# Kernel optimization log

Measured on AMD Instinct MI355X. Metric: run time of the kernel, lower is better.

Reference implementation:

```python
import jax, jax.numpy as jnp
import numpy as np

EPS_LN = 1e-6
EPS_NORM = 1e-12
MAX_SCALE_MUL = float(np.log(100.0))
H = 16  # num_heads


def _ln(x):
    # affine-free LayerNorm over last dim (torch uses biased variance)
    mu = jnp.mean(x, axis=-1, keepdims=True)
    var = jnp.mean((x - mu) ** 2, axis=-1, keepdims=True)
    return (x - mu) / jnp.sqrt(var + EPS_LN)


def _l2norm(x):
    n = jnp.sqrt(jnp.sum(x * x, axis=-1, keepdims=True))
    return x / jnp.maximum(n, EPS_NORM)


def setup_inputs() -> dict:
    key = jax.random.key(0)
    ks = jax.random.split(key, 12)
    B, L, C = 4, 1024, 1024
    Ccond, Dff = 1024, 4096
    s = lambda fan: 1.0 / np.sqrt(fan)
    return {
        "x": jax.random.normal(ks[0], (B, L, C), jnp.float32),
        "cond": jax.random.normal(ks[1], (B, Ccond), jnp.float32),
        "mat_qkv_w": jax.random.normal(ks[2], (3 * C, C), jnp.float32) * s(C),
        "q_bias": jnp.zeros((C,), jnp.float32),
        "v_bias": jnp.zeros((C,), jnp.float32),
        "scale_mul": jnp.full((1, H, 1, 1), np.log(4.0), jnp.float32),
        "proj_w": jax.random.normal(ks[3], (C, C), jnp.float32) * s(C),
        "proj_b": jnp.zeros((C,), jnp.float32),
        "ada_w": jax.random.normal(ks[4], (6 * C, Ccond), jnp.float32) * s(Ccond),
        "ada_b": jnp.zeros((6 * C,), jnp.float32),
        "fc1_w": jax.random.normal(ks[5], (Dff, C), jnp.float32) * s(C),
        "fc1_b": jnp.zeros((Dff,), jnp.float32),
        "fc2_w": jax.random.normal(ks[6], (C, Dff), jnp.float32) * s(Dff),
        "fc2_b": jnp.zeros((C,), jnp.float32),
    }


def reference(x, cond, mat_qkv_w, q_bias, v_bias, scale_mul, proj_w, proj_b,
              ada_w, ada_b, fc1_w, fc1_b, fc2_w, fc2_b):
    B, L, C = x.shape
    hd = C // H

    # AdaLN modulation params: SiLU -> Linear -> [B,1,6,C]
    ada = jax.nn.silu(cond) @ ada_w.T + ada_b
    ada = ada.reshape(B, 1, 6, C)
    gamma1, gamma2, scale1, scale2, shift1, shift2 = [ada[:, :, i] for i in range(6)]

    # --- attention branch ---
    x1 = _ln(x) * (scale1 + 1.0) + shift1
    qkv_bias = jnp.concatenate([q_bias, jnp.zeros_like(q_bias), v_bias])
    qkv = (x1 @ mat_qkv_w.T + qkv_bias).reshape(B, L, 3, H, hd)
    q, k, v = [jnp.transpose(qkv[:, :, i], (0, 2, 1, 3)) for i in range(3)]  # [B,H,L,hd]

    sm = jnp.exp(jnp.minimum(scale_mul, MAX_SCALE_MUL))  # [1,H,1,1]
    q = _l2norm(q) * sm
    k = _l2norm(k)

    scores = jnp.einsum('bhqd,bhkd->bhqk', q, k)  # scale = 1.0 under l2 norm
    probs = jax.nn.softmax(scores, axis=-1)
    o = jnp.einsum('bhqk,bhkd->bhqd', probs, v)
    o = jnp.transpose(o, (0, 2, 1, 3)).reshape(B, L, C)
    attn_out = o @ proj_w.T + proj_b
    x = x + attn_out * gamma1

    # --- FFN branch ---
    x2 = _ln(x) * (scale2 + 1.0) + shift2
    h = jax.nn.gelu(x2 @ fc1_w.T + fc1_b, approximate=False)
    ffn_out = h @ fc2_w.T + fc2_b
    x = x + ffn_out * gamma2
    return x
```

## Files before the change

### kernel.cpp

```cpp
#include <hip/hip_runtime.h>

typedef __bf16 bf16x8_t __attribute__((ext_vector_type(8)));
typedef bf16x8_t bf16x8 __attribute__((may_alias));
typedef float f32x4 __attribute__((ext_vector_type(4)));
typedef unsigned short u16x4 __attribute__((ext_vector_type(4)));
typedef unsigned short u16x8 __attribute__((ext_vector_type(8)));

#define DEV __device__ __forceinline__

DEV float b2f(unsigned short u) {
  union { unsigned int i; float f; } x; x.i = ((unsigned int)u) << 16; return x.f;
}
DEV unsigned short f2b(float f) {
  union { float f; unsigned int i; } x; x.f = f;
  return (unsigned short)((x.i + 0x7fffu + ((x.i >> 16) & 1u)) >> 16);
}

#define AS1(p) ((__attribute__((address_space(1))) void*)(p))
#define AS3(p) ((__attribute__((address_space(3))) void*)(p))

__global__ void k_silu(const float* __restrict__ c, float* __restrict__ o) {
  int i = blockIdx.x * 256 + threadIdx.x;
  float v = c[i];
  o[i] = v / (1.f + __expf(-v));
}

__global__ __launch_bounds__(256) void k_ada(const float* __restrict__ sc,
                                             const float* __restrict__ w,
                                             const float* __restrict__ bias,
                                             float* __restrict__ out) {
  int j = blockIdx.x * 4 + (threadIdx.x >> 6);
  int lane = threadIdx.x & 63;
  const float* wr = w + (size_t)j * 1024;
  float s0 = 0.f, s1 = 0.f, s2 = 0.f, s3 = 0.f;
#pragma unroll
  for (int u = 0; u < 4; ++u) {
    int k = u * 256 + lane * 4;
    float4 a = *(const float4*)(wr + k);
    float4 c0 = *(const float4*)(sc + k);
    float4 c1 = *(const float4*)(sc + 1024 + k);
    float4 c2 = *(const float4*)(sc + 2048 + k);
    float4 c3 = *(const float4*)(sc + 3072 + k);
    s0 += a.x * c0.x + a.y * c0.y + a.z * c0.z + a.w * c0.w;
    s1 += a.x * c1.x + a.y * c1.y + a.z * c1.z + a.w * c1.w;
    s2 += a.x * c2.x + a.y * c2.y + a.z * c2.z + a.w * c2.w;
    s3 += a.x * c3.x + a.y * c3.y + a.z * c3.z + a.w * c3.w;
  }
#pragma unroll
  for (int o = 1; o < 64; o <<= 1) {
    s0 += __shfl_xor(s0, o); s1 += __shfl_xor(s1, o);
    s2 += __shfl_xor(s2, o); s3 += __shfl_xor(s3, o);
  }
  if (lane == 0) {
    float bb = bias[j];
    out[j] = s0 + bb;
    out[6144 + j] = s1 + bb;
    out[12288 + j] = s2 + bb;
    out[18432 + j] = s3 + bb;
  }
}

__global__ void k_cast(const float* __restrict__ s, unsigned short* __restrict__ d, int n) {
  int i = (blockIdx.x * 256 + threadIdx.x) * 4;
  if (i >= n) return;
  float4 v = *(const float4*)(s + i);
  u16x4 o;
  o[0] = f2b(v.x); o[1] = f2b(v.y); o[2] = f2b(v.z); o[3] = f2b(v.w);
  *(u16x4*)(d + i) = o;
}

__global__ __launch_bounds__(256) void k_ln_mod(const float* __restrict__ src,
                                                const float* __restrict__ ada,
                                                unsigned short* __restrict__ dst,
                                                int sidx, int hidx) {
  int row = blockIdx.x;
  int b = row >> 10;
  int t = threadIdx.x, lane = t & 63, wv = t >> 6;
  float4 v = *(const float4*)(src + (size_t)row * 1024 + t * 4);
  float s = v.x + v.y + v.z + v.w;
  float s2 = v.x * v.x + v.y * v.y + v.z * v.z + v.w * v.w;
#pragma unroll
  for (int o = 1; o < 64; o <<= 1) { s += __shfl_xor(s, o); s2 += __shfl_xor(s2, o); }
  __shared__ float red[8];
  if (lane == 0) { red[wv] = s; red[4 + wv] = s2; }
  __syncthreads();
  float ts = red[0] + red[1] + red[2] + red[3];
  float ts2 = red[4] + red[5] + red[6] + red[7];
  float mu = ts * (1.f / 1024.f);
  float var = ts2 * (1.f / 1024.f) - mu * mu;
  float rstd = rsqrtf(var + 1e-6f);
  const float* ar = ada + (size_t)b * 6144;
  float4 sc = *(const float4*)(ar + sidx * 1024 + t * 4);
  float4 sh = *(const float4*)(ar + hidx * 1024 + t * 4);
  u16x4 o;
  o[0] = f2b((v.x - mu) * rstd * (sc.x + 1.f) + sh.x);
  o[1] = f2b((v.y - mu) * rstd * (sc.y + 1.f) + sh.y);
  o[2] = f2b((v.z - mu) * rstd * (sc.z + 1.f) + sh.z);
  o[3] = f2b((v.w - mu) * rstd * (sc.w + 1.f) + sh.w);
  *(u16x4*)(dst + (size_t)row * 1024 + t * 4) = o;
}

template <int EPI, int SPLIT>
__global__ __launch_bounds__(512, 2) void k_gemm256(const unsigned short* __restrict__ A,
                                                    const unsigned short* __restrict__ W,
                                                    int N, int lda, int ldb, int nt,
                                                    const float* __restrict__ bias,
                                                    const float* __restrict__ qb,
                                                    const float* __restrict__ vb,
                                                    unsigned short* __restrict__ o0,
                                                    unsigned short* __restrict__ o1,
                                                    unsigned short* __restrict__ o2,
                                                    unsigned short* __restrict__ o3) {
  __shared__ unsigned short LDS[65536];
  const int tid = threadIdx.x;
  const int wv = tid >> 6, lane = tid & 63;
  const int fr = lane & 15, fg = lane >> 4;
  const int wm = wv >> 2, wn = wv & 3;

  const int cpx = gridDim.x >> 3;
  int wid = ((int)blockIdx.x & 7) * cpx + ((int)blockIdx.x >> 3);
  int s = 0;
  if (SPLIT > 1) { s = wid & (SPLIT - 1); wid >>= 2; }
  const int nx = N >> 8;
  const int m0 = (wid / nx) * 256, n0 = (wid % nx) * 256;
  const int kbase = s * (nt << 6);
  unsigned short* outp = (SPLIT > 1) ? (s == 0 ? o0 : s == 1 ? o1 : s == 2 ? o2 : o3) : o0;

  const int sRow = lane >> 2;
  const int sCh = (lane & 3) ^ ((lane >> 3) & 3);
  const unsigned short* aG = A + (size_t)(m0 + wv * 16 + sRow) * lda + kbase + sCh * 8;
  const unsigned short* bG = W + (size_t)(n0 + wv * 16 + sRow) * ldb + kbase + sCh * 8;

#define STQ(qi_, iop_, rh_)                                                                   \
  __builtin_amdgcn_global_load_lds(                                                          \
      AS1(((iop_) ? bG : aG) + (size_t)(rh_)*128 * ((iop_) ? ldb : lda) +                    \
          (((qi_) >> 1) * 64 + ((qi_)&1) * 32)),                                             \
      AS3(LDS + ((qi_)&3) * 16384 + (iop_)*8192 + (rh_)*4096 + wv * 512), 16, 0, 0)

  const int rswz = (fr >> 1) & 3;
  const int aRd = (wm * 128 + fr) * 32 + ((fg ^ rswz) << 3);
  const int bRd = 8192 + (wn * 64 + fr) * 32 + ((fg ^ rswz) << 3);

  f32x4 zz = {0.f, 0.f, 0.f, 0.f};
  f32x4 acc[8][4];
#pragma unroll
  for (int i = 0; i < 8; ++i)
#pragma unroll
    for (int j = 0; j < 4; ++j) acc[i][j] = zz;

#pragma unroll
  for (int qq = 0; qq < 3; ++qq) {
    STQ(qq, 0, 0); STQ(qq, 0, 1); STQ(qq, 1, 0); STQ(qq, 1, 1);
  }
  asm volatile("s_waitcnt vmcnt(8)" ::: "memory");
  __builtin_amdgcn_s_barrier();

#define LDSV(off) (*(const bf16x8*)(LDS + (off)))

  for (int t = 0; t < nt; ++t) {
    bf16x8 bq0, bq1, bq2, bq3;
#pragma unroll
    for (int p = 0; p < 4; ++p) {
      const int kk = p >> 1;
      const int reg = ((2 * t + kk) & 3) * 16384;
      if ((p & 1) == 0) {
        bq0 = LDSV(reg + bRd);
        bq1 = LDSV(reg + bRd + 512);
        bq2 = LDSV(reg + bRd + 1024);
        bq3 = LDSV(reg + bRd + 1536);
      }
      bf16x8 a0 = LDSV(reg + aRd + (p & 1) * 2048);
      bf16x8 a1 = LDSV(reg + aRd + (p & 1) * 2048 + 512);
      bf16x8 a2 = LDSV(reg + aRd + (p & 1) * 2048 + 1024);
      bf16x8 a3 = LDSV(reg + aRd + (p & 1) * 2048 + 1536);
      {
        const int gph = 4 * t + p;
        const int qi = (gph >> 1) + 3;
        if (qi < 2 * nt) {
          const int iop = gph & 1;
          if (iop) { STQ(qi, 1, 0); STQ(qi, 1, 1); }
          else     { STQ(qi, 0, 0); STQ(qi, 0, 1); }
        }
      }
      __builtin_amdgcn_s_barrier();
      asm volatile("s_waitcnt lgkmcnt(0)" ::: "memory");
      __builtin_amdgcn_sched_barrier(0);
      __builtin_amdgcn_s_setprio(1);
      const int mg = (p & 1) * 4;
#pragma unroll
      for (int ni = 0; ni < 4; ++ni) {
        bf16x8 bb = ni == 0 ? bq0 : ni == 1 ? bq1 : ni == 2 ? bq2 : bq3;
        acc[mg + 0][ni] = __builtin_amdgcn_mfma_f32_16x16x32_bf16(a0, bb, acc[mg + 0][ni], 0, 0, 0);
        acc[mg + 1][ni] = __builtin_amdgcn_mfma_f32_16x16x32_bf16(a1, bb, acc[mg + 1][ni], 0, 0, 0);
        acc[mg + 2][ni] = __builtin_amdgcn_mfma_f32_16x16x32_bf16(a2, bb, acc[mg + 2][ni], 0, 0, 0);
        acc[mg + 3][ni] = __builtin_amdgcn_mfma_f32_16x16x32_bf16(a3, bb, acc[mg + 3][ni], 0, 0, 0);
      }
      __builtin_amdgcn_s_setprio(0);
      if (p == 1) {
        if (t == nt - 1) { asm volatile("s_waitcnt vmcnt(0)" ::: "memory"); }
        else             { asm volatile("s_waitcnt vmcnt(8)" ::: "memory"); }
      } else if (p == 3 && t < nt - 1) {
        if (t == nt - 2) { asm volatile("s_waitcnt vmcnt(4)" ::: "memory"); }
        else             { asm volatile("s_waitcnt vmcnt(8)" ::: "memory"); }
      }
      __builtin_amdgcn_s_barrier();
    }
  }

#pragma unroll
  for (int mi = 0; mi < 8; ++mi) {
#pragma unroll
    for (int ni = 0; ni < 4; ++ni) {
#pragma unroll
      for (int r = 0; r < 4; ++r) {
        int m = m0 + wm * 128 + mi * 16 + fg * 4 + r;
        int n = n0 + wn * 64 + ni * 16 + fr;
        float v = acc[mi][ni][r];
        if constexpr (EPI == 0) {
          float bb = (n < 1024) ? qb[n] : ((n < 2048) ? 0.f : vb[n - 2048]);
          outp[(size_t)m * N + n] = f2b(v + bb);
        } else if constexpr (EPI == 2) {
          float z = v + bias[n];
          float u = z * (0.7978845608f + 0.0356774081f * z * z);
          float e = __expf(2.f * u);
          float th = 1.f - 2.f / (e + 1.f);
          outp[(size_t)m * N + n] = f2b(0.5f * z * (1.f + th));
        } else {
          outp[(size_t)m * N + n] = f2b(v);
        }
      }
    }
  }
#undef STQ
#undef LDSV
}

__global__ __launch_bounds__(256) void k_fc2red(const unsigned short* __restrict__ P0,
                                                const unsigned short* __restrict__ P1,
                                                const unsigned short* __restrict__ P2,
                                                const unsigned short* __restrict__ P3,
                                                const float* __restrict__ xmid,
                                                const float* __restrict__ bias,
                                                const float* __restrict__ ada,
                                                float* __restrict__ out) {
  size_t idx = ((size_t)blockIdx.x * 256 + threadIdx.x) * 8;
  int n = (int)(idx & 1023);
  int b = (int)(idx >> 20);
  u16x8 v0 = *(const u16x8*)(P0 + idx);
  u16x8 v1 = *(const u16x8*)(P1 + idx);
  u16x8 v2 = *(const u16x8*)(P2 + idx);
  u16x8 v3 = *(const u16x8*)(P3 + idx);
  const float* gp = ada + (size_t)b * 6144 + 1024 + n;
  const float* bp = bias + n;
  const float* xp = xmid + idx;
  float* op = out + idx;
#pragma unroll
  for (int i = 0; i < 8; ++i) {
    float sum = b2f(v0[i]) + b2f(v1[i]) + b2f(v2[i]) + b2f(v3[i]);
    op[i] = xp[i] + (sum + bp[i]) * gp[i];
  }
}

__global__ __launch_bounds__(512) void k_gemm8(const unsigned short* __restrict__ A,
                                               const unsigned short* __restrict__ W,
                                               int M, int N, int K, int Khalf,
                                               const float* __restrict__ bias,
                                               const float* __restrict__ resid,
                                               const float* __restrict__ ada,
                                               float* __restrict__ outp) {
  __shared__ unsigned short SM[49152];
  const int t = threadIdx.x, lane = t & 63, wv = t >> 6;
  const int grp = wv >> 2, w4 = wv & 3;
  const int wr = w4 >> 1, wc = w4 & 1;
  const int cpx = gridDim.x >> 3;
  const int orig = blockIdx.x;
  const int wid = (orig & 7) * cpx + (orig >> 3);
  const int nx = N >> 7;
  const int m0 = (wid / nx) * 128, n0 = (wid % nx) * 128;

  f32x4 zz = {0.f, 0.f, 0.f, 0.f};
  f32x4 acc[4][4];
#pragma unroll
  for (int i = 0; i < 4; ++i)
#pragma unroll
    for (int j = 0; j < 4; ++j) acc[i][j] = zz;

  const int srow = lane >> 2, scol = (lane & 3) * 8;
  const int kbase = grp * Khalf;
  const unsigned short* aSrc0 = A + (size_t)(m0 + w4 * 16 + srow) * K + kbase + scol;
  const unsigned short* aSrc1 = aSrc0 + (size_t)64 * K;
  const unsigned short* bSrc0 = W + (size_t)(n0 + w4 * 16 + srow) * K + kbase + scol;
  const unsigned short* bSrc1 = bSrc0 + (size_t)64 * K;
  unsigned short* grpA = SM + grp * 24576;

  const int fr = lane & 15, fk = (lane >> 4) * 8;

#define STG8(buf_, k0_)                                                                            \
  {                                                                                                \
    __builtin_amdgcn_global_load_lds(AS1(aSrc0 + (k0_)), AS3(grpA + (buf_)*8192 + w4 * 512), 16, 0, 0); \
    __builtin_amdgcn_global_load_lds(AS1(aSrc1 + (k0_)), AS3(grpA + (buf_)*8192 + 2048 + w4 * 512), 16, 0, 0); \
    __builtin_amdgcn_global_load_lds(AS1(bSrc0 + (k0_)), AS3(grpA + (buf_)*8192 + 4096 + w4 * 512), 16, 0, 0); \
    __builtin_amdgcn_global_load_lds(AS1(bSrc1 + (k0_)), AS3(grpA + (buf_)*8192 + 6144 + w4 * 512), 16, 0, 0); \
  }

  const int nsteps = Khalf >> 5;
  STG8(0, 0);
  STG8(1, 32);
  asm volatile("s_waitcnt vmcnt(4)" ::: "memory");
  __builtin_amdgcn_s_barrier();

  for (int i = 0; i < nsteps; ++i) {
    const int buf = i % 3;
    if (i + 2 < nsteps) STG8((i + 2) % 3, (i + 2) * 32);
    const unsigned short* aRd = grpA + buf * 8192 + (wr * 64 + fr) * 32 + fk;
    const unsigned short* bRd = grpA + buf * 8192 + 4096 + (wc * 64 + fr) * 32 + fk;
    bf16x8 af[4], bfv[4];
#pragma unroll
    for (int q = 0; q < 4; ++q) af[q] = *(const bf16x8*)(aRd + q * 512);
#pragma unroll
    for (int q = 0; q < 4; ++q) bfv[q] = *(const bf16x8*)(bRd + q * 512);
#pragma unroll
    for (int mi = 0; mi < 4; ++mi)
#pragma unroll
      for (int ni = 0; ni < 4; ++ni)
        acc[mi][ni] = __builtin_amdgcn_mfma_f32_16x16x32_bf16(af[mi], bfv[ni], acc[mi][ni], 0, 0, 0);
    if (i < nsteps - 1) {
      if (i + 2 < nsteps) {
        asm volatile("s_waitcnt vmcnt(4)" ::: "memory");
      } else {
        asm volatile("s_waitcnt vmcnt(0)" ::: "memory");
      }
      __builtin_amdgcn_s_barrier();
    }
  }
  __syncthreads();

  float* xch = (float*)SM;
#pragma unroll
  for (int c = 0; c < 16; ++c) {
    if (grp == 1)
      *(f32x4*)&xch[c * 1024 + (w4 * 64 + lane) * 4] = acc[c >> 2][c & 3];
  }
  __syncthreads();
  if (grp == 1) return;
#pragma unroll
  for (int c = 0; c < 16; ++c) {
    f32x4 p = *(const f32x4*)&xch[c * 1024 + (w4 * 64 + lane) * 4];
    acc[c >> 2][c & 3] += p;
  }

  const int fg = lane >> 4;
#pragma unroll
  for (int mi = 0; mi < 4; ++mi) {
#pragma unroll
    for (int ni = 0; ni < 4; ++ni) {
#pragma unroll
      for (int r = 0; r < 4; ++r) {
        int m = m0 + wr * 64 + mi * 16 + fg * 4 + r;
        int n = n0 + wc * 64 + ni * 16 + fr;
        float v = acc[mi][ni][r];
        float g = ada[(size_t)(m >> 10) * 6144 + n];
        outp[(size_t)m * N + n] = resid[(size_t)m * N + n] + (v + bias[n]) * g;
      }
    }
  }
#undef STG8
}

__global__ __launch_bounds__(256) void k_qknorm(const unsigned short* __restrict__ qkv,
                                                const float* __restrict__ smul,
                                                unsigned short* __restrict__ Qn,
                                                unsigned short* __restrict__ Kn) {
  int row = blockIdx.x;
  int b = row >> 10, l = row & 1023;
  int t = threadIdx.x;
  int h = t >> 4, sl = t & 15;
  const unsigned short* base = qkv + (size_t)row * 3072 + h * 64 + sl * 4;
  size_t off = ((size_t)(b * 16 + h) * 1024 + l) * 64 + sl * 4;
  {
    u16x4 qv = *(const u16x4*)base;
    float q0 = b2f(qv[0]), q1 = b2f(qv[1]), q2 = b2f(qv[2]), q3 = b2f(qv[3]);
    float ss = q0 * q0 + q1 * q1 + q2 * q2 + q3 * q3;
#pragma unroll
    for (int o = 1; o < 16; o <<= 1) ss += __shfl_xor(ss, o);
    float sm = __expf(fminf(smul[h], 4.6051701859880914f));
    float qs = sm / fmaxf(sqrtf(ss), 1e-12f);
    u16x4 o; o[0] = f2b(q0 * qs); o[1] = f2b(q1 * qs); o[2] = f2b(q2 * qs); o[3] = f2b(q3 * qs);
    *(u16x4*)(Qn + off) = o;
  }
  {
    u16x4 kv = *(const u16x4*)(base + 1024);
    float k0 = b2f(kv[0]), k1 = b2f(kv[1]), k2 = b2f(kv[2]), k3 = b2f(kv[3]);
    float ss = k0 * k0 + k1 * k1 + k2 * k2 + k3 * k3;
#pragma unroll
    for (int o = 1; o < 16; o <<= 1) ss += __shfl_xor(ss, o);
    float ks = 1.f / fmaxf(sqrtf(ss), 1e-12f);
    u16x4 o; o[0] = f2b(k0 * ks); o[1] = f2b(k1 * ks); o[2] = f2b(k2 * ks); o[3] = f2b(k3 * ks);
    *(u16x4*)(Kn + off) = o;
  }
}

__global__ __launch_bounds__(256) void k_vtrans(const unsigned short* __restrict__ qkv,
                                                unsigned short* __restrict__ Vt) {
  int bh = blockIdx.y, b = bh >> 4, h = bh & 15;
  int l0 = blockIdx.x * 64;
  __shared__ unsigned short tile[64][72];
  int t = threadIdx.x;
  int lr = t >> 2, dp = (t & 3) * 16;
  const unsigned short* src = qkv + (size_t)(b * 1024 + l0 + lr) * 3072 + 2048 + h * 64 + dp;
  *(u16x8*)&tile[lr][dp] = *(const u16x8*)src;
  *(u16x8*)&tile[lr][dp + 8] = *(const u16x8*)(src + 8);
  __syncthreads();
  int d = t >> 2, lp = (t & 3) * 16;
  unsigned short ov[16];
#pragma unroll
  for (int j = 0; j < 16; ++j) {
    int p = lp + j;
    int l = ((p >> 5) * 2 + ((p >> 2) & 1)) * 16 + ((p >> 3) & 3) * 4 + (p & 3);
    ov[j] = tile[l][d];
  }
  unsigned short* dst = Vt + ((size_t)bh * 64 + d) * 1024 + l0 + lp;
  *(u16x8*)dst = *(u16x8*)&ov[0];
  *(u16x8*)(dst + 8) = *(u16x8*)&ov[8];
}

__global__ __launch_bounds__(256) void k_attn(const unsigned short* __restrict__ Qn,
                                              const unsigned short* __restrict__ Kn,
                                              const unsigned short* __restrict__ Vt,
                                              const float* __restrict__ smul,
                                              unsigned short* __restrict__ O) {
  const int qt = blockIdx.x, bh = blockIdx.y;
  const int b = bh >> 4, h = bh & 15;
  const int t = threadIdx.x, lane = t & 63, wv = t >> 6;
  const int fr = lane & 15, fg = lane >> 4;
  __shared__ unsigned short Kb[2][4096];
  __shared__ unsigned short Vb[2][4096];

  const int q0 = qt * 128 + wv * 32;
  const unsigned short* qp = Qn + ((size_t)bh * 1024 + q0 + fr) * 64 + fg * 8;
  bf16x8 qf00 = *(const bf16x8*)qp;
  bf16x8 qf01 = *(const bf16x8*)(qp + 32);
  bf16x8 qf10 = *(const bf16x8*)(qp + 1024);
  bf16x8 qf11 = *(const bf16x8*)(qp + 1024 + 32);

  const float M = __expf(fminf(smul[h], 4.6051701859880914f));

  const int srow = lane >> 3, sc = lane & 7;
  const int xr = (sc ^ srow) * 8;
  const unsigned short* kp0 = Kn + (size_t)bh * 65536 + (size_t)(wv * 16 + srow) * 64 + xr;
  const unsigned short* kp1 = kp0 + 8 * 64;
  const unsigned short* vp0 = Vt + (size_t)bh * 65536 + (size_t)(wv * 16 + srow) * 1024 + xr;
  const unsigned short* vp1 = vp0 + 8 * 1024;

  f32x4 zz = {0.f, 0.f, 0.f, 0.f};
  f32x4 oa0[4], oa1[4];
#pragma unroll
  for (int i = 0; i < 4; ++i) { oa0[i] = zz; oa1[i] = zz; }
  float ls0 = 0.f, ls1 = 0.f;

  {
    unsigned short* kd = &Kb[0][wv * 1024];
    unsigned short* vd = &Vb[0][wv * 1024];
    __builtin_amdgcn_global_load_lds(AS1(kp0), AS3(kd), 16, 0, 0);
    __builtin_amdgcn_global_load_lds(AS1(kp1), AS3(kd + 512), 16, 0, 0);
    __builtin_amdgcn_global_load_lds(AS1(vp0), AS3(vd), 16, 0, 0);
    __builtin_amdgcn_global_load_lds(AS1(vp1), AS3(vd + 512), 16, 0, 0);
  }
  __syncthreads();

  int cur = 0;
  for (int kv = 0; kv < 1024; kv += 64) {
    const int nxt = cur ^ 1;
    if (kv + 64 < 1024) {
      const int ko = (kv + 64) * 64;
      const int vo = kv + 64;
      unsigned short* kd = &Kb[nxt][wv * 1024];
      unsigned short* vd = &Vb[nxt][wv * 1024];
      __builtin_amdgcn_global_load_lds(AS1(kp0 + ko), AS3(kd), 16, 0, 0);
      __builtin_amdgcn_global_load_lds(AS1(kp1 + ko), AS3(kd + 512), 16, 0, 0);
      __builtin_amdgcn_global_load_lds(AS1(vp0 + vo), AS3(vd), 16, 0, 0);
      __builtin_amdgcn_global_load_lds(AS1(vp1 + vo), AS3(vd + 512), 16, 0, 0);
    }

    f32x4 s0[4], s1[4];
#pragma unroll
    for (int ct = 0; ct < 4; ++ct) {
      const int row = ct * 16 + fr, r7 = row & 7;
      const unsigned short* kr = &Kb[cur][row * 64];
      bf16x8 kf0 = *(const bf16x8*)(kr + ((fg ^ r7) << 3));
      bf16x8 kf1 = *(const bf16x8*)(kr + (((4 + fg) ^ r7) << 3));
      f32x4 z0 = __builtin_amdgcn_mfma_f32_16x16x32_bf16(kf0, qf00, zz, 0, 0, 0);
      s0[ct] = __builtin_amdgcn_mfma_f32_16x16x32_bf16(kf1, qf01, z0, 0, 0, 0);
      f32x4 z1 = __builtin_amdgcn_mfma_f32_16x16x32_bf16(kf0, qf10, zz, 0, 0, 0);
      s1[ct] = __builtin_amdgcn_mfma_f32_16x16x32_bf16(kf1, qf11, z1, 0, 0, 0);
    }

    bf16x8 pa0[2], pa1[2];
#pragma unroll
    for (int kg = 0; kg < 2; ++kg) {
      bf16x8 a0, a1;
#pragma unroll
      for (int c2 = 0; c2 < 2; ++c2) {
#pragma unroll
        for (int r = 0; r < 4; ++r) {
          float e0 = __expf(s0[kg * 2 + c2][r] - M);
          float e1 = __expf(s1[kg * 2 + c2][r] - M);
          ls0 += e0; ls1 += e1;
          a0[c2 * 4 + r] = (__bf16)e0;
          a1[c2 * 4 + r] = (__bf16)e1;
        }
      }
      pa0[kg] = a0; pa1[kg] = a1;
    }

#pragma unroll
    for (int kg = 0; kg < 2; ++kg) {
#pragma unroll
      for (int dt = 0; dt < 4; ++dt) {
        const int row = dt * 16 + fr, r7 = row & 7;
        bf16x8 vf = *(const bf16x8*)(&Vb[cur][row * 64] + ((((kg << 2) + fg) ^ r7) << 3));
        oa0[dt] = __builtin_amdgcn_mfma_f32_16x16x32_bf16(pa0[kg], vf, oa0[dt], 0, 0, 0);
        oa1[dt] = __builtin_amdgcn_mfma_f32_16x16x32_bf16(pa1[kg], vf, oa1[dt], 0, 0, 0);
      }
    }
    __syncthreads();
    cur = nxt;
  }

  ls0 += __shfl_xor(ls0, 16); ls0 += __shfl_xor(ls0, 32);
  ls1 += __shfl_xor(ls1, 16); ls1 += __shfl_xor(ls1, 32);

#pragma unroll
  for (int r = 0; r < 4; ++r) {
    float i0 = 1.f / __shfl(ls0, fg * 4 + r);
    float i1 = 1.f / __shfl(ls1, fg * 4 + r);
    unsigned short* ob = O + ((size_t)(b * 1024 + q0 + fg * 4 + r)) * 1024 + h * 64 + fr;
#pragma unroll
    for (int dt = 0; dt < 4; ++dt) {
      ob[dt * 16] = f2b(oa0[dt][r] * i0);
      ob[(size_t)16 * 1024 + dt * 16] = f2b(oa1[dt][r] * i1);
    }
  }
}

extern "C" void kernel_launch(void* const* d_in, const int* in_sizes, int n_in,
                              void* d_out, int out_size, void* d_ws, size_t ws_size,
                              hipStream_t stream) {
  const float* x        = (const float*)d_in[0];
  const float* cond     = (const float*)d_in[1];
  const float* qkv_w    = (const float*)d_in[2];
  const float* q_bias   = (const float*)d_in[3];
  const float* v_bias   = (const float*)d_in[4];
  const float* scale_mul= (const float*)d_in[5];
  const float* proj_w   = (const float*)d_in[6];
  const float* proj_b   = (const float*)d_in[7];
  const float* ada_w    = (const float*)d_in[8];
  const float* ada_b    = (const float*)d_in[9];
  const float* fc1_w    = (const float*)d_in[10];
  const float* fc1_b    = (const float*)d_in[11];
  const float* fc2_w    = (const float*)d_in[12];
  const float* fc2_b    = (const float*)d_in[13];
  float* out = (float*)d_out;
  char* ws = (char*)d_ws;

  unsigned short* WQ   = (unsigned short*)(ws + 0);
  unsigned short* WP   = (unsigned short*)(ws + 6291456);
  unsigned short* WF1  = (unsigned short*)(ws + 8388608);
  unsigned short* WF2  = (unsigned short*)(ws + 16777216);
  float*          SIL  = (float*)(ws + 25165824);
  float*          ADA  = (float*)(ws + 25182208);
  unsigned short* X1   = (unsigned short*)(ws + 25280512);
  unsigned short* QKVB = (unsigned short*)(ws + 33669120);
  unsigned short* QN   = (unsigned short*)(ws + 58834944);
  unsigned short* KN   = (unsigned short*)(ws + 67223552);
  unsigned short* VT   = (unsigned short*)(ws + 75612160);
  unsigned short* OB   = (unsigned short*)(ws + 84000768);
  float*          XMID = (float*)(ws + 33669120);
  unsigned short* HB   = (unsigned short*)(ws + 50446336);
  unsigned short* FP0  = (unsigned short*)(ws + 0);
  unsigned short* FP1  = (unsigned short*)(ws + 8388608);
  unsigned short* FP2  = (unsigned short*)(ws + 25280512);
  unsigned short* FP3  = (unsigned short*)(ws + 84000768);

  (void)in_sizes; (void)n_in; (void)out_size; (void)ws_size;

  k_silu<<<16, 256, 0, stream>>>(cond, SIL);
  k_ada<<<1536, 256, 0, stream>>>(SIL, ada_w, ada_b, ADA);
  k_cast<<<3072, 256, 0, stream>>>(qkv_w, WQ, 3145728);
  k_cast<<<1024, 256, 0, stream>>>(proj_w, WP, 1048576);
  k_cast<<<4096, 256, 0, stream>>>(fc1_w, WF1, 4194304);
  k_cast<<<4096, 256, 0, stream>>>(fc2_w, WF2, 4194304);

  k_ln_mod<<<4096, 256, 0, stream>>>(x, ADA, X1, 2, 4);
  k_gemm256<0, 1><<<192, 512, 0, stream>>>(X1, WQ, 3072, 1024, 1024, 16,
                                           nullptr, q_bias, v_bias, QKVB, nullptr, nullptr, nullptr);
  k_qknorm<<<4096, 256, 0, stream>>>(QKVB, scale_mul, QN, KN);
  k_vtrans<<<dim3(16, 64), 256, 0, stream>>>(QKVB, VT);
  k_attn<<<dim3(8, 64), 256, 0, stream>>>(QN, KN, VT, scale_mul, OB);
  k_gemm8<<<256, 512, 0, stream>>>(OB, WP, 4096, 1024, 1024, 512,
                                   proj_b, x, ADA, XMID);
  k_ln_mod<<<4096, 256, 0, stream>>>(XMID, ADA, X1, 3, 5);
  k_gemm256<2, 1><<<256, 512, 0, stream>>>(X1, WF1, 4096, 1024, 1024, 16,
                                           fc1_b, nullptr, nullptr, HB, nullptr, nullptr, nullptr);
  k_gemm256<4, 4><<<256, 512, 0, stream>>>(HB, WF2, 1024, 4096, 4096, 16,
                                           nullptr, nullptr, nullptr, FP0, FP1, FP2, FP3);
  k_fc2red<<<2048, 256, 0, stream>>>(FP0, FP1, FP2, FP3, XMID, fc2_b, ADA, out);
}
```

Measured before the change: 237.8 us.

## Simplify GEMM pipeline to one barrier per stage and fuse prologue kernels

The bf16 GEMM main loop is restructured so each K-stage issues one batch of four global-to-LDS loads three stages ahead. It then reads all A and B fragments and runs the 32 MFMAs, with a single barrier per stage. This replaces the previous two-phase interleaving, which used setprio and two barriers per phase. Launch bounds are relaxed to one block per SM. The prologue is also trimmed: SiLU is fused into the AdaLN projection kernel, and the four weight-cast kernels are merged into one launch. The aim is to cut synchronisation and launch overhead, at the risk of losing the finer load/MFMA overlap and of each AdaLN block redundantly recomputing SiLU over the whole condition vector.

```diff
diff --git a/kernel.cpp b/kernel.cpp
--- a/kernel.cpp
+++ b/kernel.cpp
@@ -19,18 +19,20 @@
 #define AS1(p) ((__attribute__((address_space(1))) void*)(p))
 #define AS3(p) ((__attribute__((address_space(3))) void*)(p))
 
-__global__ void k_silu(const float* __restrict__ c, float* __restrict__ o) {
-  int i = blockIdx.x * 256 + threadIdx.x;
-  float v = c[i];
-  o[i] = v / (1.f + __expf(-v));
-}
-
-__global__ __launch_bounds__(256) void k_ada(const float* __restrict__ sc,
+__global__ __launch_bounds__(256) void k_ada(const float* __restrict__ cond,
                                              const float* __restrict__ w,
                                              const float* __restrict__ bias,
                                              float* __restrict__ out) {
-  int j = blockIdx.x * 4 + (threadIdx.x >> 6);
-  int lane = threadIdx.x & 63;
+  __shared__ float sc[4096];
+  int tt = threadIdx.x;
+#pragma unroll
+  for (int i = 0; i < 16; ++i) {
+    float v = cond[tt + i * 256];
+    sc[tt + i * 256] = v / (1.f + __expf(-v));
+  }
+  __syncthreads();
+  int j = blockIdx.x * 4 + (tt >> 6);
+  int lane = tt & 63;
   const float* wr = w + (size_t)j * 1024;
   float s0 = 0.f, s1 = 0.f, s2 = 0.f, s3 = 0.f;
 #pragma unroll
@@ -60,13 +62,26 @@
   }
 }
 
-__global__ void k_cast(const float* __restrict__ s, unsigned short* __restrict__ d, int n) {
-  int i = (blockIdx.x * 256 + threadIdx.x) * 4;
-  if (i >= n) return;
-  float4 v = *(const float4*)(s + i);
-  u16x4 o;
-  o[0] = f2b(v.x); o[1] = f2b(v.y); o[2] = f2b(v.z); o[3] = f2b(v.w);
-  *(u16x4*)(d + i) = o;
+__global__ __launch_bounds__(256) void k_castall(const float* __restrict__ q,
+                                                 const float* __restrict__ p,
+                                                 const float* __restrict__ f1,
+                                                 const float* __restrict__ f2,
+                                                 unsigned short* __restrict__ wq,
+                                                 unsigned short* __restrict__ wp,
+                                                 unsigned short* __restrict__ wf1,
+                                                 unsigned short* __restrict__ wf2) {
+  int i = blockIdx.x * 256 + threadIdx.x;
+  for (int v = i; v < 3145728; v += 524288) {
+    const float* s; unsigned short* d; int off;
+    if (v < 786432) { s = q; d = wq; off = v; }
+    else if (v < 1048576) { s = p; d = wp; off = v - 786432; }
+    else if (v < 2097152) { s = f1; d = wf1; off = v - 1048576; }
+    else { s = f2; d = wf2; off = v - 2097152; }
+    float4 x = ((const float4*)s)[off];
+    u16x4 o;
+    o[0] = f2b(x.x); o[1] = f2b(x.y); o[2] = f2b(x.z); o[3] = f2b(x.w);
+    *(u16x4*)(d + (size_t)off * 4) = o;
+  }
 }
 
 __global__ __launch_bounds__(256) void k_ln_mod(const float* __restrict__ src,
@@ -101,7 +116,7 @@
 }
 
 template <int EPI, int SPLIT>
-__global__ __launch_bounds__(512, 2) void k_gemm256(const unsigned short* __restrict__ A,
+__global__ __launch_bounds__(512, 1) void k_gemm256(const unsigned short* __restrict__ A,
                                                     const unsigned short* __restrict__ W,
                                                     int N, int lda, int ldb, int nt,
                                                     const float* __restrict__ bias,
@@ -119,27 +134,33 @@
 
   const int cpx = gridDim.x >> 3;
   int wid = ((int)blockIdx.x & 7) * cpx + ((int)blockIdx.x >> 3);
-  int s = 0;
-  if (SPLIT > 1) { s = wid & (SPLIT - 1); wid >>= 2; }
+  int sp = 0;
+  if (SPLIT > 1) { sp = wid & (SPLIT - 1); wid >>= 2; }
   const int nx = N >> 8;
   const int m0 = (wid / nx) * 256, n0 = (wid % nx) * 256;
-  const int kbase = s * (nt << 6);
-  unsigned short* outp = (SPLIT > 1) ? (s == 0 ? o0 : s == 1 ? o1 : s == 2 ? o2 : o3) : o0;
+  const int kbase = sp * (nt << 6);
+  unsigned short* outp = (SPLIT > 1) ? (sp == 0 ? o0 : sp == 1 ? o1 : sp == 2 ? o2 : o3) : o0;
 
   const int sRow = lane >> 2;
   const int sCh = (lane & 3) ^ ((lane >> 3) & 3);
   const unsigned short* aG = A + (size_t)(m0 + wv * 16 + sRow) * lda + kbase + sCh * 8;
   const unsigned short* bG = W + (size_t)(n0 + wv * 16 + sRow) * ldb + kbase + sCh * 8;
 
-#define STQ(qi_, iop_, rh_)                                                                   \
-  __builtin_amdgcn_global_load_lds(                                                          \
-      AS1(((iop_) ? bG : aG) + (size_t)(rh_)*128 * ((iop_) ? ldb : lda) +                    \
-          (((qi_) >> 1) * 64 + ((qi_)&1) * 32)),                                             \
-      AS3(LDS + ((qi_)&3) * 16384 + (iop_)*8192 + (rh_)*4096 + wv * 512), 16, 0, 0)
+#define STQ4(qi_)                                                                              \
+  {                                                                                            \
+    const int wr_ = ((qi_)&3) * 16384;                                                         \
+    const int ko_ = (qi_)*32;                                                                  \
+    __builtin_amdgcn_global_load_lds(AS1(aG + ko_), AS3(LDS + wr_ + wv * 512), 16, 0, 0);      \
+    __builtin_amdgcn_global_load_lds(AS1(aG + (size_t)128 * lda + ko_),                        \
+                                     AS3(LDS + wr_ + 4096 + wv * 512), 16, 0, 0);              \
+    __builtin_amdgcn_global_load_lds(AS1(bG + ko_), AS3(LDS + wr_ + 8192 + wv * 512), 16, 0, 0);\
+    __builtin_amdgcn_global_load_lds(AS1(bG + (size_t)128 * ldb + ko_),                        \
+                                     AS3(LDS + wr_ + 12288 + wv * 512), 16, 0, 0);             \
+  }
 
   const int rswz = (fr >> 1) & 3;
-  const int aRd = (wm * 128 + fr) * 32 + ((fg ^ rswz) << 3);
-  const int bRd = 8192 + (wn * 64 + fr) * 32 + ((fg ^ rswz) << 3);
+  const int aOff = (wm * 128 + fr) * 32 + ((fg ^ rswz) << 3);
+  const int bOff = 8192 + (wn * 64 + fr) * 32 + ((fg ^ rswz) << 3);
 
   f32x4 zz = {0.f, 0.f, 0.f, 0.f};
   f32x4 acc[8][4];
@@ -149,62 +170,38 @@
     for (int j = 0; j < 4; ++j) acc[i][j] = zz;
 
 #pragma unroll
-  for (int qq = 0; qq < 3; ++qq) {
-    STQ(qq, 0, 0); STQ(qq, 0, 1); STQ(qq, 1, 0); STQ(qq, 1, 1);
-  }
+  for (int q = 0; q < 3; ++q) STQ4(q);
   asm volatile("s_waitcnt vmcnt(8)" ::: "memory");
   __builtin_amdgcn_s_barrier();
 
 #define LDSV(off) (*(const bf16x8*)(LDS + (off)))
 
-  for (int t = 0; t < nt; ++t) {
-    bf16x8 bq0, bq1, bq2, bq3;
-#pragma unroll
-    for (int p = 0; p < 4; ++p) {
-      const int kk = p >> 1;
-      const int reg = ((2 * t + kk) & 3) * 16384;
-      if ((p & 1) == 0) {
-        bq0 = LDSV(reg + bRd);
-        bq1 = LDSV(reg + bRd + 512);
-        bq2 = LDSV(reg + bRd + 1024);
-        bq3 = LDSV(reg + bRd + 1536);
-      }
-      bf16x8 a0 = LDSV(reg + aRd + (p & 1) * 2048);
-      bf16x8 a1 = LDSV(reg + aRd + (p & 1) * 2048 + 512);
-      bf16x8 a2 = LDSV(reg + aRd + (p & 1) * 2048 + 1024);
-      bf16x8 a3 = LDSV(reg + aRd + (p & 1) * 2048 + 1536);
-      {
-        const int gph = 4 * t + p;
-        const int qi = (gph >> 1) + 3;
-        if (qi < 2 * nt) {
-          const int iop = gph & 1;
-          if (iop) { STQ(qi, 1, 0); STQ(qi, 1, 1); }
-          else     { STQ(qi, 0, 0); STQ(qi, 0, 1); }
-        }
-      }
-      __builtin_amdgcn_s_barrier();
-      asm volatile("s_waitcnt lgkmcnt(0)" ::: "memory");
-      __builtin_amdgcn_sched_barrier(0);
-      __builtin_amdgcn_s_setprio(1);
-      const int mg = (p & 1) * 4;
-#pragma unroll
-      for (int ni = 0; ni < 4; ++ni) {
-        bf16x8 bb = ni == 0 ? bq0 : ni == 1 ? bq1 : ni == 2 ? bq2 : bq3;
-        acc[mg + 0][ni] = __builtin_amdgcn_mfma_f32_16x16x32_bf16(a0, bb, acc[mg + 0][ni], 0, 0, 0);
-        acc[mg + 1][ni] = __builtin_amdgcn_mfma_f32_16x16x32_bf16(a1, bb, acc[mg + 1][ni], 0, 0, 0);
-        acc[mg + 2][ni] = __builtin_amdgcn_mfma_f32_16x16x32_bf16(a2, bb, acc[mg + 2][ni], 0, 0, 0);
-        acc[mg + 3][ni] = __builtin_amdgcn_mfma_f32_16x16x32_bf16(a3, bb, acc[mg + 3][ni], 0, 0, 0);
-      }
-      __builtin_amdgcn_s_setprio(0);
-      if (p == 1) {
-        if (t == nt - 1) { asm volatile("s_waitcnt vmcnt(0)" ::: "memory"); }
-        else             { asm volatile("s_waitcnt vmcnt(8)" ::: "memory"); }
-      } else if (p == 3 && t < nt - 1) {
-        if (t == nt - 2) { asm volatile("s_waitcnt vmcnt(4)" ::: "memory"); }
-        else             { asm volatile("s_waitcnt vmcnt(8)" ::: "memory"); }
-      }
-      __builtin_amdgcn_s_barrier();
-    }
+  const int ns = 2 * nt;
+  for (int st = 0; st < ns; ++st) {
+    if (st + 3 < ns) STQ4(st + 3);
+    const int rb = (st & 3) * 16384;
+    bf16x8 bf0 = LDSV(rb + bOff);
+    bf16x8 bf1 = LDSV(rb + bOff + 512);
+    bf16x8 bf2 = LDSV(rb + bOff + 1024);
+    bf16x8 bf3 = LDSV(rb + bOff + 1536);
+    bf16x8 af[8];
+#pragma unroll
+    for (int mi = 0; mi < 8; ++mi) af[mi] = LDSV(rb + aOff + mi * 512);
+#pragma unroll
+    for (int mi = 0; mi < 8; ++mi) {
+      acc[mi][0] = __builtin_amdgcn_mfma_f32_16x16x32_bf16(af[mi], bf0, acc[mi][0], 0, 0, 0);
+      acc[mi][1] = __builtin_amdgcn_mfma_f32_16x16x32_bf16(af[mi], bf1, acc[mi][1], 0, 0, 0);
+      acc[mi][2] = __builtin_amdgcn_mfma_f32_16x16x32_bf16(af[mi], bf2, acc[mi][2], 0, 0, 0);
+      acc[mi][3] = __builtin_amdgcn_mfma_f32_16x16x32_bf16(af[mi], bf3, acc[mi][3], 0, 0, 0);
+    }
+    if (st < ns - 3) {
+      asm volatile("s_waitcnt vmcnt(8)" ::: "memory");
+    } else if (st == ns - 3) {
+      asm volatile("s_waitcnt vmcnt(4)" ::: "memory");
+    } else if (st == ns - 2) {
+      asm volatile("s_waitcnt vmcnt(0)" ::: "memory");
+    }
+    __builtin_amdgcn_s_barrier();
   }
 
 #pragma unroll
@@ -231,7 +228,7 @@
       }
     }
   }
-#undef STQ
+#undef STQ4
 #undef LDSV
 }
 
@@ -567,7 +564,6 @@
   unsigned short* WP   = (unsigned short*)(ws + 6291456);
   unsigned short* WF1  = (unsigned short*)(ws + 8388608);
   unsigned short* WF2  = (unsigned short*)(ws + 16777216);
-  float*          SIL  = (float*)(ws + 25165824);
   float*          ADA  = (float*)(ws + 25182208);
   unsigned short* X1   = (unsigned short*)(ws + 25280512);
   unsigned short* QKVB = (unsigned short*)(ws + 33669120);
@@ -584,12 +580,8 @@
 
   (void)in_sizes; (void)n_in; (void)out_size; (void)ws_size;
 
-  k_silu<<<16, 256, 0, stream>>>(cond, SIL);
-  k_ada<<<1536, 256, 0, stream>>>(SIL, ada_w, ada_b, ADA);
-  k_cast<<<3072, 256, 0, stream>>>(qkv_w, WQ, 3145728);
-  k_cast<<<1024, 256, 0, stream>>>(proj_w, WP, 1048576);
-  k_cast<<<4096, 256, 0, stream>>>(fc1_w, WF1, 4194304);
-  k_cast<<<4096, 256, 0, stream>>>(fc2_w, WF2, 4194304);
+  k_ada<<<1536, 256, 0, stream>>>(cond, ada_w, ada_b, ADA);
+  k_castall<<<2048, 256, 0, stream>>>(qkv_w, proj_w, fc1_w, fc2_w, WQ, WP, WF1, WF2);
 
   k_ln_mod<<<4096, 256, 0, stream>>>(x, ADA, X1, 2, 4);
   k_gemm256<0, 1><<<192, 512, 0, stream>>>(X1, WQ, 3072, 1024, 1024, 16,
```

After: 227.6 us. 1.04x faster.
